# Kernel tuning notes

Measured on AMD Instinct MI355X. Metric: run time of the kernel, lower is better.

## Reference

```python
import jax, jax.numpy as jnp
import numpy as np

B, S, D, E, TOP_K = 4, 4096, 2048, 64, 8


def setup_inputs() -> dict:
    key = jax.random.key(0)
    k1, k2, k3, k4 = jax.random.split(key, 4)
    scale = 1.0 / np.sqrt(D)
    return {
        "x": jax.random.normal(k1, (B, S, D), dtype=jnp.float32),
        "noise": jax.random.normal(k2, (B, S, E), dtype=jnp.float32),
        "W_route": jax.random.normal(k3, (D, E), dtype=jnp.float32) * scale,
        "b_route": jnp.zeros((E,), dtype=jnp.float32),
        "W_noise": jax.random.normal(k4, (D, E), dtype=jnp.float32) * scale,
        "b_noise": jnp.zeros((E,), dtype=jnp.float32),
    }


def reference(x, noise, W_route, b_route, W_noise, b_noise):
    # logits / noise_logits: [B, S, E]
    logits = jnp.einsum("bsd,de->bse", x, W_route) + b_route
    noise_logits = jnp.einsum("bsd,de->bse", x, W_noise) + b_noise
    noisy_logits = logits + noise * jax.nn.softplus(noise_logits)

    topk_vals, topk_idx = jax.lax.top_k(noisy_logits, TOP_K)  # [B,S,K]
    # softmax over -inf-masked logits == softmax over topk values scattered
    # into a zero tensor (non-selected experts get exactly 0 probability).
    topk_probs = jax.nn.softmax(topk_vals, axis=-1)  # [B,S,K]

    flat_idx = topk_idx.reshape(B * S, TOP_K)
    flat_probs = topk_probs.reshape(B * S, TOP_K)
    rows = jnp.arange(B * S)[:, None]
    router_output = (
        jnp.zeros((B * S, E), dtype=topk_probs.dtype)
        .at[rows, flat_idx].set(flat_probs)
        .reshape(B, S, E)
    )
    return router_output, topk_idx
```

## Files before the change

kernel.cpp:

```cpp
#include <hip/hip_runtime.h>
#include <hip/hip_bf16.h>
#include <math.h>


#define BD 2048
#define BE 64
#define RPW 8
#define WPB 4
#define ROWS_PER_BLOCK (RPW * WPB)

__global__ __launch_bounds__(256, 2)
void noisy_topk_router(const float* __restrict__ x,
                       const float* __restrict__ noise,
                       const float* __restrict__ Wr,
                       const float* __restrict__ brp,
                       const float* __restrict__ Wn,
                       const float* __restrict__ bnp,
                       float* __restrict__ out,
                       int BS)
{
    const int lane = threadIdx.x & 63;
    const int wave = threadIdx.x >> 6;
    const int m0 = __builtin_amdgcn_readfirstlane(blockIdx.x * ROWS_PER_BLOCK + wave * RPW);
    const float* xbase = x + (size_t)m0 * BD;

    const float brv = brp[lane];
    const float bnv = bnp[lane];

    double tr[RPW], tn[RPW];
#pragma unroll
    for (int i = 0; i < RPW; ++i) { tr[i] = 0.0; tn[i] = 0.0; }

    for (int dc = 0; dc < BD; dc += 128) {
        float ar[RPW], an[RPW];
#pragma unroll
        for (int i = 0; i < RPW; ++i) { ar[i] = 0.f; an[i] = 0.f; }
#pragma unroll 2
        for (int d = dc; d < dc + 128; d += 4) {
            float4 xv[RPW];
#pragma unroll
            for (int i = 0; i < RPW; ++i)
                xv[i] = *reinterpret_cast<const float4*>(xbase + (size_t)i * BD + d);
#pragma unroll
            for (int k = 0; k < 4; ++k) {
                const float wr = Wr[(d + k) * BE + lane];
                const float wn = Wn[(d + k) * BE + lane];
#pragma unroll
                for (int i = 0; i < RPW; ++i) {
                    const float xs = (k == 0) ? xv[i].x : (k == 1) ? xv[i].y
                                   : (k == 2) ? xv[i].z : xv[i].w;
                    ar[i] = fmaf(xs, wr, ar[i]);
                    an[i] = fmaf(xs, wn, an[i]);
                }
            }
        }
#pragma unroll
        for (int i = 0; i < RPW; ++i) { tr[i] += (double)ar[i]; tn[i] += (double)an[i]; }
    }

    const size_t P = (size_t)BS * BE;

#pragma unroll 1
    for (int i = 0; i < RPW; ++i) {
        const int row = m0 + i;
        const float vr = (float)tr[i] + brv;
        const float vn = (float)tn[i] + bnv;
        const float nz = noise[(size_t)row * BE + lane];
        const float sp  = fmaxf(vn, 0.f) + log1pf(expf(-fabsf(vn)));
        const float val = fmaf(nz, sp, vr);

        float cur = val;
        float bv_a[8];
        int   bi_a[8];
#pragma unroll
        for (int j = 0; j < 8; ++j) {
            float bv = cur;
            int   bi = lane;
#pragma unroll
            for (int off = 32; off > 0; off >>= 1) {
                const float ov = __shfl_xor(bv, off);
                const int   oi = __shfl_xor(bi, off);
                if (ov > bv || (ov == bv && oi < bi)) { bv = ov; bi = oi; }
            }
            bv_a[j] = bv;
            bi_a[j] = bi;
            if (lane == bi) cur = -INFINITY;
        }

        const float mx = bv_a[0];
        float p[8];
        float s = 0.f;
#pragma unroll
        for (int j = 0; j < 8; ++j) { p[j] = expf(bv_a[j] - mx); s += p[j]; }

        float myp = 0.f;
#pragma unroll
        for (int j = 0; j < 8; ++j) { if (bi_a[j] == lane) myp = p[j] / s; }

        out[(size_t)row * BE + lane] = myp;
#pragma unroll
        for (int j = 0; j < 8; ++j) {
            if (lane == j) out[P + (size_t)row * 8 + j] = (float)bi_a[j];
        }
    }
}

extern "C" void kernel_launch(void* const* d_in, const int* in_sizes, int n_in,
                              void* d_out, int out_size, void* d_ws, size_t ws_size,
                              hipStream_t stream) {
    (void)n_in; (void)d_ws; (void)ws_size; (void)out_size;
    const float* x     = (const float*)d_in[0];
    const float* noise = (const float*)d_in[1];
    const float* Wr    = (const float*)d_in[2];
    const float* br    = (const float*)d_in[3];
    const float* Wn    = (const float*)d_in[4];
    const float* bn    = (const float*)d_in[5];
    float* out = (float*)d_out;

    const int BS = in_sizes[1] / BE;
    const int blocks = BS / ROWS_PER_BLOCK;
    noisy_topk_router<<<blocks, 256, 0, stream>>>(x, noise, Wr, br, Wn, bn, out, BS);
}
```

Measured before the change: 465.9 us.

## Split the D reduction across waves with an LDS partial-sum combine

Each block now handles 8 rows, and its 4 waves each cover a quarter of the D dimension instead of owning separate rows. Per-wave partial logits go to shared memory and are summed after a barrier, and each wave then runs the top-k and softmax epilogue for 2 rows. The grid grows fourfold and launch bounds are raised to target more resident blocks, which should increase parallelism and latency hiding. The cost is extra LDS traffic, a block-wide sync, and a different summation order.

```diff
diff --git a/kernel.cpp b/kernel.cpp
--- a/kernel.cpp
+++ b/kernel.cpp
@@ -5,11 +5,11 @@
 
 #define BD 2048
 #define BE 64
-#define RPW 8
-#define WPB 4
-#define ROWS_PER_BLOCK (RPW * WPB)
+#define RPB 8
+#define NW 4
+#define DPW (BD / NW)
 
-__global__ __launch_bounds__(256, 2)
+__global__ __launch_bounds__(256, 8)
 void noisy_topk_router(const float* __restrict__ x,
                        const float* __restrict__ noise,
                        const float* __restrict__ Wr,
@@ -20,33 +20,34 @@
                        int BS)
 {
     const int lane = threadIdx.x & 63;
-    const int wave = threadIdx.x >> 6;
-    const int m0 = __builtin_amdgcn_readfirstlane(blockIdx.x * ROWS_PER_BLOCK + wave * RPW);
-    const float* xbase = x + (size_t)m0 * BD;
+    const int wave = __builtin_amdgcn_readfirstlane(threadIdx.x >> 6);
+    const int m0   = __builtin_amdgcn_readfirstlane(blockIdx.x * RPB);
+    const int d0   = wave * DPW;
+    const float* xbase = x + (size_t)m0 * BD + d0;
 
-    const float brv = brp[lane];
-    const float bnv = bnp[lane];
+    __shared__ float pr[NW][RPB][BE];
+    __shared__ float pn[NW][RPB][BE];
 
-    double tr[RPW], tn[RPW];
+    double tr[RPB], tn[RPB];
 #pragma unroll
-    for (int i = 0; i < RPW; ++i) { tr[i] = 0.0; tn[i] = 0.0; }
+    for (int i = 0; i < RPB; ++i) { tr[i] = 0.0; tn[i] = 0.0; }
 
-    for (int dc = 0; dc < BD; dc += 128) {
-        float ar[RPW], an[RPW];
+    for (int dc = 0; dc < DPW; dc += 128) {
+        float ar[RPB], an[RPB];
 #pragma unroll
-        for (int i = 0; i < RPW; ++i) { ar[i] = 0.f; an[i] = 0.f; }
+        for (int i = 0; i < RPB; ++i) { ar[i] = 0.f; an[i] = 0.f; }
 #pragma unroll 2
         for (int d = dc; d < dc + 128; d += 4) {
-            float4 xv[RPW];
+            float4 xv[RPB];
 #pragma unroll
-            for (int i = 0; i < RPW; ++i)
+            for (int i = 0; i < RPB; ++i)
                 xv[i] = *reinterpret_cast<const float4*>(xbase + (size_t)i * BD + d);
 #pragma unroll
             for (int k = 0; k < 4; ++k) {
-                const float wr = Wr[(d + k) * BE + lane];
-                const float wn = Wn[(d + k) * BE + lane];
+                const float wr = Wr[(size_t)(d0 + d + k) * BE + lane];
+                const float wn = Wn[(size_t)(d0 + d + k) * BE + lane];
 #pragma unroll
-                for (int i = 0; i < RPW; ++i) {
+                for (int i = 0; i < RPB; ++i) {
                     const float xs = (k == 0) ? xv[i].x : (k == 1) ? xv[i].y
                                    : (k == 2) ? xv[i].z : xv[i].w;
                     ar[i] = fmaf(xs, wr, ar[i]);
@@ -55,16 +56,31 @@
             }
         }
 #pragma unroll
-        for (int i = 0; i < RPW; ++i) { tr[i] += (double)ar[i]; tn[i] += (double)an[i]; }
+        for (int i = 0; i < RPB; ++i) { tr[i] += (double)ar[i]; tn[i] += (double)an[i]; }
     }
 
+#pragma unroll
+    for (int i = 0; i < RPB; ++i) {
+        pr[wave][i][lane] = (float)tr[i];
+        pn[wave][i][lane] = (float)tn[i];
+    }
+    __syncthreads();
+
+    const float brv = brp[lane];
+    const float bnv = bnp[lane];
     const size_t P = (size_t)BS * BE;
 
 #pragma unroll 1
-    for (int i = 0; i < RPW; ++i) {
-        const int row = m0 + i;
-        const float vr = (float)tr[i] + brv;
-        const float vn = (float)tn[i] + bnv;
+    for (int ii = 0; ii < RPB / NW; ++ii) {
+        const int rl  = wave * (RPB / NW) + ii;
+        const int row = m0 + rl;
+
+        double sr = 0.0, sn = 0.0;
+#pragma unroll
+        for (int w = 0; w < NW; ++w) { sr += (double)pr[w][rl][lane]; sn += (double)pn[w][rl][lane]; }
+
+        const float vr = (float)sr + brv;
+        const float vn = (float)sn + bnv;
         const float nz = noise[(size_t)row * BE + lane];
         const float sp  = fmaxf(vn, 0.f) + log1pf(expf(-fabsf(vn)));
         const float val = fmaf(nz, sp, vr);
@@ -118,6 +134,6 @@
     float* out = (float*)d_out;
 
     const int BS = in_sizes[1] / BE;
-    const int blocks = BS / ROWS_PER_BLOCK;
-    noisy_topk_router<<<blocks, 256, 0, stream>>>(x, noise, Wr, br, Wn, bn, out, BS);
+    const int blocks = BS / RPB;
+    noisy_topk_router<<<blocks, NW * 64, 0, stream>>>(x, noise, Wr, br, Wn, bn, out, BS);
 }
```

After: 446.3 us. 4.2% less time.
